# Performance work log

Measured on AMD Instinct MI355X. Metric: run time of the kernel, lower is better.

Reference implementation:

```python
import math
import jax, jax.numpy as jnp
import numpy as np

RM = 100.0      # r_max
RN = 1000       # r_dsc
LMAX = 2
MATCH_FRAC = 0.1
PARA1 = 1.0
RD = RM / RN    # radial step
NE = 4096       # batch of trial energies


def setup_inputs() -> dict:
    key = jax.random.key(0)
    # small negative energies (bound-state regime) to keep the exponential
    # Numerov growth over 900 steps within fp32 range
    init_energy = -(jax.random.uniform(key, (NE,), dtype=jnp.float32) * 0.01 + 0.005)
    return {"init_energy": init_energy}


def _disc_solve(sol0, factor, limit):
    # sol0: (5, n_e, L) initial 5-point window; factor: (rn, n_e, L)
    # Numerov-style 4-step recurrence, vectorized coefficients + lax.scan
    c = 3.0 / 40.0 * RD ** 2
    idx = jnp.arange(1, limit - 5)
    f0 = factor[idx]
    f1 = factor[idx + 1]
    f2 = factor[idx + 2]
    f3 = factor[idx + 3]
    f4 = factor[idx + 4]
    denom = 1.0 - c * f4
    a = -1.0 + c * f0 / denom
    b = 2.0 + (13.0 / 15.0) * RD ** 2 * f1 / denom
    cc = -2.0 + (7.0 / 60.0) * RD ** 2 * f2 / denom
    d = 2.0 + (13.0 / 15.0) * RD ** 2 * f3 / denom

    def step(prev, coef):
        ca, cb, ccc, cd = coef
        new4 = ca * prev[1] + cb * prev[2] + ccc * prev[3] + cd * prev[4]
        new = jnp.concatenate([prev[1:], new4[None]], axis=0)  # shift window
        return new, new

    _, rest = jax.lax.scan(step, sol0, (a, b, cc, d))
    return jnp.concatenate([sol0[None], rest], axis=0)  # (limit-5, 5, n_e, L)


def _derivative(func, at):
    return (25.0 * func[at - 1] - 48.0 * func[at - 2] + 36.0 * func[at - 3]
            - 16.0 * func[at - 4] + 3.0 * func[at - 5]) / (12.0 * RD)


def _integrate(func):
    # faithful to original: integrand squares `func` again (func is u**2 here)
    M = func.shape[0] // 4 - 1
    g0 = func[0:4 * M:4]
    g1 = func[1:4 * M:4]
    g2 = func[2:4 * M:4]
    g3 = func[3:4 * M:4]
    g4 = func[4::4][:M]
    integrand = (7.0 * (g0 ** 2 + g4 ** 2) + 32.0 * (g1 ** 2 + g3 ** 2)
                 + 12.0 * g2) * (2.0 * RD / 45.0)
    return integrand.sum(axis=0)


def _forward(init_energy):
    L = LMAX + 1
    dt = init_energy.dtype
    n_e = init_energy.shape[0]
    r = jnp.linspace(RM / RN, RM, RN, dtype=dt).reshape(RN, 1, 1)
    l = jnp.arange(L, dtype=dt).reshape(1, 1, L)

    energy = jnp.broadcast_to(init_energy[:, None], (n_e, L))  # (n_e, L)
    e_val = energy[None]                                       # (1, n_e, L)
    # coulomb potential -1/r; factor: (rn, n_e, L)
    factor = l * (l + 1) / r ** 2 + PARA1 * (-e_val - 1.0 / r)

    # left (r->0) initial window: u ~ r^(l+1) + r^(l+2)/(2(l+1)) * (-para_1)
    r0 = jnp.linspace(RD, 5 * RD, 5, dtype=dt).reshape(5, 1, 1)
    u_zero_init = jnp.broadcast_to(
        r0 ** (l + 1) - r0 ** (l + 2) / (2.0 * (l + 1)) * PARA1, (5, n_e, L))

    # right (r->r_max) initial window: r * truncated spherical-bessel series
    r_inf = jnp.linspace(RM - 4 * RD, RM, 5, dtype=dt).reshape(5, 1, 1)
    fact = jnp.array([math.prod([2 * li + 1 for li in range(lm + 1)])
                      for lm in range(L)], dtype=dt)  # [1, 3, 15]
    x = r_inf * jnp.sqrt(jnp.abs(e_val))              # (5, n_e, L)
    base = x ** l / fact
    t1 = x ** 2 / 2.0 / (2 * l + 3)
    t2 = (x ** 2 / 2.0) ** 2 / (2.0 * (2 * l + 3) * (2 * l + 5))
    u_infty_init = jnp.broadcast_to(r_inf * (base * (1.0 + t1 + t2)), (5, n_e, L))

    match = int(RN * MATCH_FRAC)  # 100
    uz = _disc_solve(u_zero_init, factor, match)                     # (95, 5, n_e, L)
    ui = _disc_solve(u_infty_init, factor[::-1], RN - match)[::-1]   # (895, 5, n_e, L)
    u_zero = jnp.concatenate([uz[0], uz[:, 4]], axis=0)    # (100, n_e, L)
    u_infty = jnp.concatenate([ui[0], ui[:, 4]], axis=0)   # (900, n_e, L)

    lfunc_in = _derivative(u_zero, match) / u_zero[-1]
    # faithful: the trailing flip acts on the energy axis of the (n_e, L) result
    lfunc_out = _derivative(u_infty[::-1], RN - match)[::-1] / u_infty[0]
    integ_in = _integrate(u_zero ** 2)
    integ_out = _integrate(u_infty ** 2)
    delta = -(lfunc_out - lfunc_in) / (integ_in / u_zero[-1] ** 2
                                       + integ_out / u_infty[0] ** 2)
    return (energy + delta, u_zero, u_infty)


def reference(init_energy):
    return _forward(init_energy)
```

## Files before the change

### kernel.cpp

```cpp
#include <hip/hip_runtime.h>


namespace {
constexpr int kNE    = 4096;
constexpr int kNCH   = kNE * 3;
constexpr int kMatch = 100;
constexpr float kC   = 3.0f / 40.0f * 0.01f;
constexpr float kK1  = 13.0f / 15.0f * 0.01f;
constexpr float kK2  = 7.0f / 60.0f * 0.01f;
constexpr int kSeg        = 32;
constexpr int kCPB        = 16;
constexpr int kZeroBlocks = kNCH / 512;
constexpr int kInfBlocks  = kNCH / kCPB;
}

__device__ __forceinline__ float rcp_f(float x) { return __builtin_amdgcn_rcpf(x); }
__device__ __forceinline__ float rcp_nr(float x) {
    float r = __builtin_amdgcn_rcpf(x);
    return fmaf(fmaf(-x, r, 1.0f), r, r);
}
__device__ __forceinline__ void nt_store(float* p, float v) {
    __builtin_nontemporal_store(v, p);
}

__global__ __launch_bounds__(512, 4) void solve_kernel(const float* __restrict__ energy,
                                                       float* __restrict__ out,
                                                       float* __restrict__ ws)
{
    __shared__ __align__(16) float gtp[908];
    __shared__ float sM[kSeg][4][kCPB][4];
    float* sF = &sM[0][0][0][0];

    const int bid = (int)blockIdx.x;
    const int tid = (int)threadIdx.x;
    float* uzero = out + kNCH;
    float* uinf  = out + kNCH + (size_t)kMatch * kNCH;

    if (bid < kZeroBlocks) {
        const int t  = bid * 512 + tid;
        const int l  = t % 3;
        const int ei = t / 3;
        const float e = energy[ei], negE = -e;
        const float ll1 = (float)(l * (l + 1));
        const float rdiv = (l == 0) ? 0.5f : ((l == 1) ? 0.25f : (1.0f/6.0f));
        float p0,p1,p2,p3,p4;
        {
            float pw[5];
            #pragma unroll
            for (int k = 0; k < 5; ++k) {
                float r = 0.1f * (float)(k + 1);
                float rl1 = (l == 0) ? r : ((l == 1) ? r*r : r*r*r);
                pw[k] = rl1 - (rl1 * r) * rdiv;
                nt_store(&uzero[(size_t)k * kNCH + t], pw[k]);
            }
            nt_store(&uzero[(size_t)5 * kNCH + t], pw[4]);
            p0=pw[0]; p1=pw[1]; p2=pw[2]; p3=pw[3]; p4=pw[4];
        }
        float acc4, acc2;
        {
            float q0=p0*p0, q1=p1*p1, q2=p2*p2, q3=p3*p3, q4=p4*p4;
            acc4 = 7.0f*q0*q0 + 32.0f*q1*q1 + 32.0f*q3*q3 + 14.0f*q4*q4 + 32.0f*q4*q4;
            acc2 = q2;
        }
        float f0, f1, f2, f3;
        {
            float i1 = rcp_f(0.2f), i2 = rcp_f(0.3f), i3 = rcp_f(0.4f), i4 = rcp_f(0.5f);
            f0 = fmaf(i1, fmaf(ll1, i1, -1.0f), negE);
            f1 = fmaf(i2, fmaf(ll1, i2, -1.0f), negE);
            f2 = fmaf(i3, fmaf(ll1, i3, -1.0f), negE);
            f3 = fmaf(i4, fmaf(ll1, i4, -1.0f), negE);
        }
        float* ptr = uzero + (size_t)6 * kNCH + t;
        #pragma unroll 4
        for (int j = 5; j <= 98; ++j) {
            float ri = rcp_f(fmaf((float)j, 0.1f, 0.1f));
            float f4 = fmaf(ri, fmaf(ll1, ri, -1.0f), negE);
            float iv = rcp_f(fmaf(-kC, f4, 1.0f));
            float a  = fmaf(kC  * f0, iv, -1.0f);
            float b  = fmaf(kK1 * f1, iv,  2.0f);
            float cc = fmaf(kK2 * f2, iv, -2.0f);
            float d  = fmaf(kK1 * f3, iv,  2.0f);
            float nw = fmaf(d, p4, fmaf(cc, p3, fmaf(b, p2, a * p1)));
            nt_store(ptr, nw); ptr += kNCH;
            float v2 = nw*nw, v4 = v2*v2;
            if (j <= 94) {
                int m = (j + 1) & 3;
                if (m == 2)      acc2 += v2;
                else if (m == 0) acc4 += 14.0f * v4;
                else             acc4 += 32.0f * v4;
            } else if (j == 95) {
                acc4 += 7.0f * v4;
            }
            f0 = f1; f1 = f2; f2 = f3; f3 = f4;
            p0 = p1; p1 = p2; p2 = p3; p3 = p4; p4 = nw;
        }
        float integ = fmaf(12.0f, acc2, acc4) * (2.0f * 0.1f / 45.0f);
        float deriv = fmaf(25.0f, p4, fmaf(-48.0f, p3, fmaf(36.0f, p2,
                      fmaf(-16.0f, p1, 3.0f * p0)))) * (1.0f / 1.2f);
        ws[2 * kNCH + t] = deriv / p4;
        ws[3 * kNCH + t] = integ / (p4 * p4);
        return;
    }

    for (int k = tid; k < 908; k += 512) {
        int j = k - 3;
        gtp[k] = (j >= 1 && j <= 898) ? rcp_nr(fmaf((float)j, -0.1f, 100.0f)) : 1.0f;
    }
    __syncthreads();

    const int b = bid - kZeroBlocks;
    const int g = tid & (kCPB - 1);
    const int s = tid >> 4;
    const int t = b * kCPB + g;
    const int l  = t % 3;
    const int ei = t / 3;
    const float e = energy[ei], negE = -e;
    const float ll1 = (float)(l * (l + 1));
    const int jstart = 5 + 28 * s;

    const float4* gq = (const float4*)(&gtp[jstart + 3]);
    float ff0, ff1, ff2, ff3;
    {
        const float4 wF = *(const float4*)(&gtp[jstart - 1]);
        ff0 = fmaf(wF.x, fmaf(ll1, wF.x, -1.0f), negE);
        ff1 = fmaf(wF.y, fmaf(ll1, wF.y, -1.0f), negE);
        ff2 = fmaf(wF.z, fmaf(ll1, wF.z, -1.0f), negE);
        ff3 = fmaf(wF.w, fmaf(ll1, wF.w, -1.0f), negE);
    }
    float F0 = ff0, F1 = ff1, F2 = ff2, F3 = ff3;

    float ca, cb, cc_, cd;
#define COEF(RI, FA,FB,FC,FD) \
    { float f4 = fmaf(RI, fmaf(ll1, RI, -1.0f), negE); \
      float x  = kC * f4; \
      float iv = fmaf(x, x, x) + 1.0f; \
      ca  = fmaf(kC  * FA, iv, -1.0f); \
      cb  = fmaf(kK1 * FB, iv,  2.0f); \
      cc_ = fmaf(kK2 * FC, iv, -2.0f); \
      cd  = fmaf(kK1 * FD, iv,  2.0f); \
      FA = f4; }

#define MSTEP(RI, FA,FB,FC,FD, RA,RB,RC,RD) \
    { COEF(RI, FA,FB,FC,FD) \
      RA[0] = fmaf(cd,RD[0], fmaf(cc_,RC[0], fmaf(cb,RB[0], ca*RA[0]))); \
      RA[1] = fmaf(cd,RD[1], fmaf(cc_,RC[1], fmaf(cb,RB[1], ca*RA[1]))); \
      RA[2] = fmaf(cd,RD[2], fmaf(cc_,RC[2], fmaf(cb,RB[2], ca*RA[2]))); \
      RA[3] = fmaf(cd,RD[3], fmaf(cc_,RC[3], fmaf(cb,RB[3], ca*RA[3]))); }

    if (s != 31) {
        float ra[4] = {1,0,0,0}, rb[4] = {0,1,0,0}, rc[4] = {0,0,1,0}, rd[4] = {0,0,0,1};
        #pragma unroll
        for (int gi = 0; gi < 7; ++gi) {
            const float4 w = gq[gi];
            MSTEP(w.x, F0,F1,F2,F3, ra,rb,rc,rd)
            MSTEP(w.y, F1,F2,F3,F0, rb,rc,rd,ra)
            MSTEP(w.z, F2,F3,F0,F1, rc,rd,ra,rb)
            MSTEP(w.w, F3,F0,F1,F2, rd,ra,rb,rc)
        }
        *(float4*)&sM[s][0][g][0] = make_float4(ra[0], ra[1], ra[2], ra[3]);
        *(float4*)&sM[s][1][g][0] = make_float4(rb[0], rb[1], rb[2], rb[3]);
        *(float4*)&sM[s][2][g][0] = make_float4(rc[0], rc[1], rc[2], rc[3]);
        *(float4*)&sM[s][3][g][0] = make_float4(rd[0], rd[1], rd[2], rd[3]);
    }
    __syncthreads();

    if (s == 0) {
        const float se  = sqrtf(fabsf(e));
        const float rfc = (l == 0) ? 1.0f : ((l == 1) ? (1.0f/3.0f) : (1.0f/15.0f));
        const float rt1 = (l == 0) ? (1.0f/3.0f) : ((l == 1) ? (1.0f/5.0f) : (1.0f/7.0f));
        const float rt2 = (l == 0) ? (1.0f/30.0f) : ((l == 1) ? (1.0f/70.0f) : (1.0f/126.0f));
        float pw[5];
        #pragma unroll
        for (int k = 0; k < 5; ++k) {
            float rinf = 99.6f + 0.1f * (float)k;
            float x  = rinf * se;
            float xl = (l == 0) ? 1.0f : ((l == 1) ? x : x * x);
            float h  = x * x * 0.5f;
            pw[k] = rinf * (xl * rfc * (1.0f + h * rt1 + (h * h) * rt2));
        }
        nt_store(&uinf[(size_t)899 * kNCH + t], pw[4]);
        float st0 = pw[1], st1 = pw[2], st2 = pw[3], st3 = pw[4];
        for (int ss = 0; ss < kSeg; ++ss) {
            if (ss < kSeg - 1) {
                float4 M0 = *(const float4*)&sM[ss][0][g][0];
                float4 M1 = *(const float4*)&sM[ss][1][g][0];
                float4 M2 = *(const float4*)&sM[ss][2][g][0];
                float4 M3 = *(const float4*)&sM[ss][3][g][0];
                *(float4*)&sM[ss][0][g][0] = make_float4(st0, st1, st2, st3);
                float n0 = fmaf(M0.w,st3, fmaf(M0.z,st2, fmaf(M0.y,st1, M0.x*st0)));
                float n1 = fmaf(M1.w,st3, fmaf(M1.z,st2, fmaf(M1.y,st1, M1.x*st0)));
                float n2 = fmaf(M2.w,st3, fmaf(M2.z,st2, fmaf(M2.y,st1, M2.x*st0)));
                float n3 = fmaf(M3.w,st3, fmaf(M3.z,st2, fmaf(M3.y,st1, M3.x*st0)));
                st0 = n0; st1 = n1; st2 = n2; st3 = n3;
            } else {
                *(float4*)&sM[ss][0][g][0] = make_float4(st0, st1, st2, st3);
            }
        }
    }
    __syncthreads();

    float W0[4] = {0.0f, 32.0f, 14.0f, 32.0f};
    float V0[4] = {1.0f, 0.0f, 0.0f, 0.0f};
    float WR[4] = {0.0f, 32.0f, 14.0f, 32.0f};
    float VR[4] = {1.0f, 0.0f, 0.0f, 0.0f};
    if (s == 0) {
        W0[0]=0.0f; V0[0]=0.0f; W0[1]=0.0f; W0[2]=7.0f; W0[3]=32.0f;
    }

    F0 = ff0; F1 = ff1; F2 = ff2; F3 = ff3;
    float p0, p1, p2, p3;
    {
        float4 P = *(const float4*)&sM[s][0][g][0];
        p0 = P.x; p1 = P.y; p2 = P.z; p3 = P.w;
    }
    float acc4 = 0.0f, acc2 = 0.0f;
    float* ptr = uinf + (size_t)(903 - jstart) * kNCH + t;
#define RSTEPW(RI, FA,FB,FC,FD, PA,PB,PC,PD, W,V,K) \
    { COEF(RI, FA,FB,FC,FD) \
      float nw = fmaf(cd,PD, fmaf(cc_,PC, fmaf(cb,PB, ca*PA))); \
      PA = nw; nt_store(ptr, nw); ptr -= kNCH; \
      float v2 = nw*nw, v4 = v2*v2; \
      acc4 = fmaf(W[K], v4, acc4); \
      acc2 = fmaf(V[K], v2, acc2); }
#define PG(G, W, V) \
    { const float4 w = gq[G]; \
      RSTEPW(w.x, F0,F1,F2,F3, p0,p1,p2,p3, W,V,0) \
      RSTEPW(w.y, F1,F2,F3,F0, p1,p2,p3,p0, W,V,1) \
      RSTEPW(w.z, F2,F3,F0,F1, p2,p3,p0,p1, W,V,2) \
      RSTEPW(w.w, F3,F0,F1,F2, p3,p0,p1,p2, W,V,3) }

    PG(0, W0, V0)
    PG(1, WR, VR) PG(2, WR, VR) PG(3, WR, VR) PG(4, WR, VR) PG(5, WR, VR)
    float h0 = p1, h1 = p2, h2 = p3;
    if (s == 31) { WR[2] = 0.0f; WR[3] = 0.0f; }
    PG(6, WR, VR)
    float h3 = p0, h4 = p1;
#undef PG
#undef RSTEPW

    {
        float2 rr; rr.x = acc4; rr.y = acc2;
        *(float2*)&sF[s * 256 + 64 + 4 * g] = rr;
    }
    __syncthreads();

    if (s == kSeg - 1) {
        float a4 = 0.0f, a2 = 0.0f;
        #pragma unroll
        for (int ss = 0; ss < kSeg; ++ss) {
            float2 rr = *(const float2*)&sF[ss * 256 + 64 + 4 * g];
            a4 += rr.x; a2 += rr.y;
        }
        nt_store(&uinf[(size_t)0 * kNCH + t], h0);
        nt_store(&uinf[(size_t)1 * kNCH + t], h1);
        nt_store(&uinf[(size_t)2 * kNCH + t], h2);
        nt_store(&uinf[(size_t)3 * kNCH + t], h3);
        nt_store(&uinf[(size_t)4 * kNCH + t], h4);
        float q0 = h0*h0, q1 = h1*h1, q2 = h2*h2, q3 = h3*h3, q4 = h4*h4;
        a4 += 7.0f*q0*q0 + 32.0f*q1*q1 + 32.0f*q3*q3 + 14.0f*q4*q4;
        a2 += q2;
        float integ = fmaf(12.0f, a2, a4) * (2.0f * 0.1f / 45.0f);
        float deriv = fmaf(25.0f, h0, fmaf(-48.0f, h1, fmaf(36.0f, h2,
                      fmaf(-16.0f, h3, 3.0f * h4)))) * (1.0f / 1.2f);
        ws[t]        = deriv / h0;
        ws[kNCH + t] = integ / (h0 * h0);
    }
#undef MSTEP
#undef COEF
}

__global__ __launch_bounds__(256) void final_kernel(const float* __restrict__ energy,
                                                    const float* __restrict__ ws,
                                                    float* __restrict__ out)
{
    int t = (int)blockIdx.x * 256 + (int)threadIdx.x;
    if (t >= kNCH) return;
    int l = t % 3, ei = t / 3;
    float lf_out = ws[(kNE - 1 - ei) * 3 + l];
    float lf_in  = ws[2 * kNCH + t];
    float den    = ws[kNCH + t] + ws[3 * kNCH + t];
    nt_store(&out[t], energy[ei] - (lf_out - lf_in) / den);
}

extern "C" void kernel_launch(void* const* d_in, const int* in_sizes, int n_in,
                              void* d_out, int out_size, void* d_ws, size_t ws_size,
                              hipStream_t stream) {
    (void)in_sizes; (void)n_in; (void)out_size; (void)ws_size;
    const float* energy = (const float*)d_in[0];
    float* out = (float*)d_out;
    float* ws  = (float*)d_ws;
    solve_kernel<<<kZeroBlocks + kInfBlocks, 512, 0, stream>>>(energy, out, ws);
    final_kernel<<<kNCH / 256, 256, 0, stream>>>(energy, ws, out);
}
```

Measured before the change: 84.53 us.

## Split segmented Numerov solve into separate stage and emit kernels

The fused solve kernel is split in two. A new stage kernel computes the per-segment transfer matrices and chains them into segment start states, which it writes into the output buffer as scratch. A second kernel reads those start states back from global memory and replays each segment to write the outputs, with the zero-side blocks moved into it. This frees shared memory and removes the serial chaining and barriers from the emit pass, at the cost of an extra launch, a recompute of the coefficient table, and a global-memory round trip for the states.

```diff
diff --git a/kernel.cpp b/kernel.cpp
--- a/kernel.cpp
+++ b/kernel.cpp
@@ -23,13 +23,118 @@
     __builtin_nontemporal_store(v, p);
 }
 
-__global__ __launch_bounds__(512, 4) void solve_kernel(const float* __restrict__ energy,
-                                                       float* __restrict__ out,
-                                                       float* __restrict__ ws)
+#define COEF(RI, FA,FB,FC,FD) \
+    { float f4 = fmaf(RI, fmaf(ll1, RI, -1.0f), negE); \
+      float x  = kC * f4; \
+      float iv = fmaf(x, x, x) + 1.0f; \
+      ca  = fmaf(kC  * FA, iv, -1.0f); \
+      cb  = fmaf(kK1 * FB, iv,  2.0f); \
+      cc_ = fmaf(kK2 * FC, iv, -2.0f); \
+      cd  = fmaf(kK1 * FD, iv,  2.0f); \
+      FA = f4; }
+
+__global__ __launch_bounds__(512, 4) void stage_kernel(const float* __restrict__ energy,
+                                                       float* __restrict__ out)
 {
     __shared__ __align__(16) float gtp[908];
     __shared__ float sM[kSeg][4][kCPB][4];
-    float* sF = &sM[0][0][0][0];
+
+    const int bid = (int)blockIdx.x;
+    const int tid = (int)threadIdx.x;
+    float* uinf  = out + kNCH + (size_t)kMatch * kNCH;
+
+    for (int k = tid; k < 908; k += 512) {
+        int j = k - 3;
+        gtp[k] = (j >= 1 && j <= 898) ? rcp_nr(fmaf((float)j, -0.1f, 100.0f)) : 1.0f;
+    }
+    __syncthreads();
+
+    const int g = tid & (kCPB - 1);
+    const int s = tid >> 4;
+    const int t = bid * kCPB + g;
+    const int l  = t % 3;
+    const int ei = t / 3;
+    const float e = energy[ei], negE = -e;
+    const float ll1 = (float)(l * (l + 1));
+    const int jstart = 5 + 28 * s;
+
+    const float4* gq = (const float4*)(&gtp[jstart + 3]);
+    float F0, F1, F2, F3;
+    {
+        const float4 wF = *(const float4*)(&gtp[jstart - 1]);
+        F0 = fmaf(wF.x, fmaf(ll1, wF.x, -1.0f), negE);
+        F1 = fmaf(wF.y, fmaf(ll1, wF.y, -1.0f), negE);
+        F2 = fmaf(wF.z, fmaf(ll1, wF.z, -1.0f), negE);
+        F3 = fmaf(wF.w, fmaf(ll1, wF.w, -1.0f), negE);
+    }
+    float ca, cb, cc_, cd;
+
+#define MSTEP(RI, FA,FB,FC,FD, RA,RB,RC,RD) \
+    { COEF(RI, FA,FB,FC,FD) \
+      RA[0] = fmaf(cd,RD[0], fmaf(cc_,RC[0], fmaf(cb,RB[0], ca*RA[0]))); \
+      RA[1] = fmaf(cd,RD[1], fmaf(cc_,RC[1], fmaf(cb,RB[1], ca*RA[1]))); \
+      RA[2] = fmaf(cd,RD[2], fmaf(cc_,RC[2], fmaf(cb,RB[2], ca*RA[2]))); \
+      RA[3] = fmaf(cd,RD[3], fmaf(cc_,RC[3], fmaf(cb,RB[3], ca*RA[3]))); }
+
+    if (s != 31) {
+        float ra[4] = {1,0,0,0}, rb[4] = {0,1,0,0}, rc[4] = {0,0,1,0}, rd[4] = {0,0,0,1};
+        #pragma unroll
+        for (int gi = 0; gi < 7; ++gi) {
+            const float4 w = gq[gi];
+            MSTEP(w.x, F0,F1,F2,F3, ra,rb,rc,rd)
+            MSTEP(w.y, F1,F2,F3,F0, rb,rc,rd,ra)
+            MSTEP(w.z, F2,F3,F0,F1, rc,rd,ra,rb)
+            MSTEP(w.w, F3,F0,F1,F2, rd,ra,rb,rc)
+        }
+        *(float4*)&sM[s][0][g][0] = make_float4(ra[0], ra[1], ra[2], ra[3]);
+        *(float4*)&sM[s][1][g][0] = make_float4(rb[0], rb[1], rb[2], rb[3]);
+        *(float4*)&sM[s][2][g][0] = make_float4(rc[0], rc[1], rc[2], rc[3]);
+        *(float4*)&sM[s][3][g][0] = make_float4(rd[0], rd[1], rd[2], rd[3]);
+    }
+#undef MSTEP
+    __syncthreads();
+
+    if (s == 0) {
+        const float se  = sqrtf(fabsf(e));
+        const float rfc = (l == 0) ? 1.0f : ((l == 1) ? (1.0f/3.0f) : (1.0f/15.0f));
+        const float rt1 = (l == 0) ? (1.0f/3.0f) : ((l == 1) ? (1.0f/5.0f) : (1.0f/7.0f));
+        const float rt2 = (l == 0) ? (1.0f/30.0f) : ((l == 1) ? (1.0f/70.0f) : (1.0f/126.0f));
+        float pw[5];
+        #pragma unroll
+        for (int k = 0; k < 5; ++k) {
+            float rinf = 99.6f + 0.1f * (float)k;
+            float x  = rinf * se;
+            float xl = (l == 0) ? 1.0f : ((l == 1) ? x : x * x);
+            float h  = x * x * 0.5f;
+            pw[k] = rinf * (xl * rfc * (1.0f + h * rt1 + (h * h) * rt2));
+        }
+        float st0 = pw[1], st1 = pw[2], st2 = pw[3], st3 = pw[4];
+        for (int ss = 0; ss < kSeg; ++ss) {
+            uinf[(size_t)(ss * 4 + 0) * kNCH + t] = st0;
+            uinf[(size_t)(ss * 4 + 1) * kNCH + t] = st1;
+            uinf[(size_t)(ss * 4 + 2) * kNCH + t] = st2;
+            uinf[(size_t)(ss * 4 + 3) * kNCH + t] = st3;
+            if (ss < kSeg - 1) {
+                float4 M0 = *(const float4*)&sM[ss][0][g][0];
+                float4 M1 = *(const float4*)&sM[ss][1][g][0];
+                float4 M2 = *(const float4*)&sM[ss][2][g][0];
+                float4 M3 = *(const float4*)&sM[ss][3][g][0];
+                float n0 = fmaf(M0.w,st3, fmaf(M0.z,st2, fmaf(M0.y,st1, M0.x*st0)));
+                float n1 = fmaf(M1.w,st3, fmaf(M1.z,st2, fmaf(M1.y,st1, M1.x*st0)));
+                float n2 = fmaf(M2.w,st3, fmaf(M2.z,st2, fmaf(M2.y,st1, M2.x*st0)));
+                float n3 = fmaf(M3.w,st3, fmaf(M3.z,st2, fmaf(M3.y,st1, M3.x*st0)));
+                st0 = n0; st1 = n1; st2 = n2; st3 = n3;
+            }
+        }
+    }
+}
+
+__global__ __launch_bounds__(512, 4) void emit_kernel(const float* __restrict__ energy,
+                                                      float* __restrict__ out,
+                                                      float* __restrict__ ws)
+{
+    __shared__ __align__(16) float gtp[908];
+    __shared__ float2 sRed[kSeg][kCPB];
 
     const int bid = (int)blockIdx.x;
     const int tid = (int)threadIdx.x;
@@ -102,12 +207,6 @@
         return;
     }
 
-    for (int k = tid; k < 908; k += 512) {
-        int j = k - 3;
-        gtp[k] = (j >= 1 && j <= 898) ? rcp_nr(fmaf((float)j, -0.1f, 100.0f)) : 1.0f;
-    }
-    __syncthreads();
-
     const int b = bid - kZeroBlocks;
     const int g = tid & (kCPB - 1);
     const int s = tid >> 4;
@@ -118,86 +217,27 @@
     const float ll1 = (float)(l * (l + 1));
     const int jstart = 5 + 28 * s;
 
+    float p0 = uinf[(size_t)(s * 4 + 0) * kNCH + t];
+    float p1 = uinf[(size_t)(s * 4 + 1) * kNCH + t];
+    float p2 = uinf[(size_t)(s * 4 + 2) * kNCH + t];
+    float p3 = uinf[(size_t)(s * 4 + 3) * kNCH + t];
+
+    for (int k = tid; k < 908; k += 512) {
+        int j = k - 3;
+        gtp[k] = (j >= 1 && j <= 898) ? rcp_nr(fmaf((float)j, -0.1f, 100.0f)) : 1.0f;
+    }
+    __syncthreads();
+
     const float4* gq = (const float4*)(&gtp[jstart + 3]);
-    float ff0, ff1, ff2, ff3;
+    float F0, F1, F2, F3;
     {
         const float4 wF = *(const float4*)(&gtp[jstart - 1]);
-        ff0 = fmaf(wF.x, fmaf(ll1, wF.x, -1.0f), negE);
-        ff1 = fmaf(wF.y, fmaf(ll1, wF.y, -1.0f), negE);
-        ff2 = fmaf(wF.z, fmaf(ll1, wF.z, -1.0f), negE);
-        ff3 = fmaf(wF.w, fmaf(ll1, wF.w, -1.0f), negE);
-    }
-    float F0 = ff0, F1 = ff1, F2 = ff2, F3 = ff3;
-
+        F0 = fmaf(wF.x, fmaf(ll1, wF.x, -1.0f), negE);
+        F1 = fmaf(wF.y, fmaf(ll1, wF.y, -1.0f), negE);
+        F2 = fmaf(wF.z, fmaf(ll1, wF.z, -1.0f), negE);
+        F3 = fmaf(wF.w, fmaf(ll1, wF.w, -1.0f), negE);
+    }
     float ca, cb, cc_, cd;
-#define COEF(RI, FA,FB,FC,FD) \
-    { float f4 = fmaf(RI, fmaf(ll1, RI, -1.0f), negE); \
-      float x  = kC * f4; \
-      float iv = fmaf(x, x, x) + 1.0f; \
-      ca  = fmaf(kC  * FA, iv, -1.0f); \
-      cb  = fmaf(kK1 * FB, iv,  2.0f); \
-      cc_ = fmaf(kK2 * FC, iv, -2.0f); \
-      cd  = fmaf(kK1 * FD, iv,  2.0f); \
-      FA = f4; }
-
-#define MSTEP(RI, FA,FB,FC,FD, RA,RB,RC,RD) \
-    { COEF(RI, FA,FB,FC,FD) \
-      RA[0] = fmaf(cd,RD[0], fmaf(cc_,RC[0], fmaf(cb,RB[0], ca*RA[0]))); \
-      RA[1] = fmaf(cd,RD[1], fmaf(cc_,RC[1], fmaf(cb,RB[1], ca*RA[1]))); \
-      RA[2] = fmaf(cd,RD[2], fmaf(cc_,RC[2], fmaf(cb,RB[2], ca*RA[2]))); \
-      RA[3] = fmaf(cd,RD[3], fmaf(cc_,RC[3], fmaf(cb,RB[3], ca*RA[3]))); }
-
-    if (s != 31) {
-        float ra[4] = {1,0,0,0}, rb[4] = {0,1,0,0}, rc[4] = {0,0,1,0}, rd[4] = {0,0,0,1};
-        #pragma unroll
-        for (int gi = 0; gi < 7; ++gi) {
-            const float4 w = gq[gi];
-            MSTEP(w.x, F0,F1,F2,F3, ra,rb,rc,rd)
-            MSTEP(w.y, F1,F2,F3,F0, rb,rc,rd,ra)
-            MSTEP(w.z, F2,F3,F0,F1, rc,rd,ra,rb)
-            MSTEP(w.w, F3,F0,F1,F2, rd,ra,rb,rc)
-        }
-        *(float4*)&sM[s][0][g][0] = make_float4(ra[0], ra[1], ra[2], ra[3]);
-        *(float4*)&sM[s][1][g][0] = make_float4(rb[0], rb[1], rb[2], rb[3]);
-        *(float4*)&sM[s][2][g][0] = make_float4(rc[0], rc[1], rc[2], rc[3]);
-        *(float4*)&sM[s][3][g][0] = make_float4(rd[0], rd[1], rd[2], rd[3]);
-    }
-    __syncthreads();
-
-    if (s == 0) {
-        const float se  = sqrtf(fabsf(e));
-        const float rfc = (l == 0) ? 1.0f : ((l == 1) ? (1.0f/3.0f) : (1.0f/15.0f));
-        const float rt1 = (l == 0) ? (1.0f/3.0f) : ((l == 1) ? (1.0f/5.0f) : (1.0f/7.0f));
-        const float rt2 = (l == 0) ? (1.0f/30.0f) : ((l == 1) ? (1.0f/70.0f) : (1.0f/126.0f));
-        float pw[5];
-        #pragma unroll
-        for (int k = 0; k < 5; ++k) {
-            float rinf = 99.6f + 0.1f * (float)k;
-            float x  = rinf * se;
-            float xl = (l == 0) ? 1.0f : ((l == 1) ? x : x * x);
-            float h  = x * x * 0.5f;
-            pw[k] = rinf * (xl * rfc * (1.0f + h * rt1 + (h * h) * rt2));
-        }
-        nt_store(&uinf[(size_t)899 * kNCH + t], pw[4]);
-        float st0 = pw[1], st1 = pw[2], st2 = pw[3], st3 = pw[4];
-        for (int ss = 0; ss < kSeg; ++ss) {
-            if (ss < kSeg - 1) {
-                float4 M0 = *(const float4*)&sM[ss][0][g][0];
-                float4 M1 = *(const float4*)&sM[ss][1][g][0];
-                float4 M2 = *(const float4*)&sM[ss][2][g][0];
-                float4 M3 = *(const float4*)&sM[ss][3][g][0];
-                *(float4*)&sM[ss][0][g][0] = make_float4(st0, st1, st2, st3);
-                float n0 = fmaf(M0.w,st3, fmaf(M0.z,st2, fmaf(M0.y,st1, M0.x*st0)));
-                float n1 = fmaf(M1.w,st3, fmaf(M1.z,st2, fmaf(M1.y,st1, M1.x*st0)));
-                float n2 = fmaf(M2.w,st3, fmaf(M2.z,st2, fmaf(M2.y,st1, M2.x*st0)));
-                float n3 = fmaf(M3.w,st3, fmaf(M3.z,st2, fmaf(M3.y,st1, M3.x*st0)));
-                st0 = n0; st1 = n1; st2 = n2; st3 = n3;
-            } else {
-                *(float4*)&sM[ss][0][g][0] = make_float4(st0, st1, st2, st3);
-            }
-        }
-    }
-    __syncthreads();
 
     float W0[4] = {0.0f, 32.0f, 14.0f, 32.0f};
     float V0[4] = {1.0f, 0.0f, 0.0f, 0.0f};
@@ -205,14 +245,9 @@
     float VR[4] = {1.0f, 0.0f, 0.0f, 0.0f};
     if (s == 0) {
         W0[0]=0.0f; V0[0]=0.0f; W0[1]=0.0f; W0[2]=7.0f; W0[3]=32.0f;
-    }
-
-    F0 = ff0; F1 = ff1; F2 = ff2; F3 = ff3;
-    float p0, p1, p2, p3;
-    {
-        float4 P = *(const float4*)&sM[s][0][g][0];
-        p0 = P.x; p1 = P.y; p2 = P.z; p3 = P.w;
-    }
+        nt_store(&uinf[(size_t)899 * kNCH + t], p3);
+    }
+
     float acc4 = 0.0f, acc2 = 0.0f;
     float* ptr = uinf + (size_t)(903 - jstart) * kNCH + t;
 #define RSTEPW(RI, FA,FB,FC,FD, PA,PB,PC,PD, W,V,K) \
@@ -238,17 +273,14 @@
 #undef PG
 #undef RSTEPW
 
-    {
-        float2 rr; rr.x = acc4; rr.y = acc2;
-        *(float2*)&sF[s * 256 + 64 + 4 * g] = rr;
-    }
+    sRed[s][g] = make_float2(acc4, acc2);
     __syncthreads();
 
     if (s == kSeg - 1) {
         float a4 = 0.0f, a2 = 0.0f;
         #pragma unroll
         for (int ss = 0; ss < kSeg; ++ss) {
-            float2 rr = *(const float2*)&sF[ss * 256 + 64 + 4 * g];
+            float2 rr = sRed[ss][g];
             a4 += rr.x; a2 += rr.y;
         }
         nt_store(&uinf[(size_t)0 * kNCH + t], h0);
@@ -265,8 +297,6 @@
         ws[t]        = deriv / h0;
         ws[kNCH + t] = integ / (h0 * h0);
     }
-#undef MSTEP
-#undef COEF
 }
 
 __global__ __launch_bounds__(256) void final_kernel(const float* __restrict__ energy,
@@ -289,6 +319,7 @@
     const float* energy = (const float*)d_in[0];
     float* out = (float*)d_out;
     float* ws  = (float*)d_ws;
-    solve_kernel<<<kZeroBlocks + kInfBlocks, 512, 0, stream>>>(energy, out, ws);
+    stage_kernel<<<kInfBlocks, 512, 0, stream>>>(energy, out);
+    emit_kernel<<<kZeroBlocks + kInfBlocks, 512, 0, stream>>>(energy, out, ws);
     final_kernel<<<kNCH / 256, 256, 0, stream>>>(energy, ws, out);
 }
```

After: 95.06 us. 12.5% more time.
